# Kernel optimization log

Measured on AMD Instinct MI355X. Metric: run time of the kernel, lower is better.

## Reference

```python
import jax, jax.numpy as jnp
import numpy as np

H = 512  # hidden size (layer_size in the torch module)


def setup_inputs() -> dict:
    key = jax.random.key(0)
    ks = jax.random.split(key, 12)
    B, T = 512, 128
    s = 1.0 / np.sqrt(H)  # torch default LSTM/Linear init range
    def u(k, shape):
        return jax.random.uniform(k, shape, jnp.float32, -s, s)
    return {
        "x": jax.random.normal(ks[0], (B, T, 1), jnp.float32),
        "x_time": jax.random.normal(ks[1], (B, T), jnp.float32),
        "y_time": jax.random.normal(ks[2], (B, T), jnp.float32),
        # layer 0: input_size=1
        "w_ih0": u(ks[3], (4 * H, 1)),
        "w_hh0": u(ks[4], (4 * H, H)),
        "b_ih0": u(ks[5], (4 * H,)),
        "b_hh0": u(ks[6], (4 * H,)),
        # layer 1: input_size=H
        "w_ih1": u(ks[7], (4 * H, H)),
        "w_hh1": u(ks[8], (4 * H, H)),
        "b_ih1": u(ks[9], (4 * H,)),
        "b_hh1": u(ks[10], (4 * H,)),
        # output head Linear(512, 1)
        "w_lin": u(ks[11], (1, H)),
        "b_lin": jnp.zeros((1,), jnp.float32),
    }


def _cell(x, h, c, w_ih, w_hh, b):
    # torch LSTM gate order: i, f, g, o
    g = x @ w_ih.T + h @ w_hh.T + b
    i, f, gg, o = jnp.split(g, 4, axis=-1)
    c = jax.nn.sigmoid(f) * c + jax.nn.sigmoid(i) * jnp.tanh(gg)
    h = jax.nn.sigmoid(o) * jnp.tanh(c)
    return h, c


def reference(x, x_time, y_time, w_ih0, w_hh0, b_ih0, b_hh0,
              w_ih1, w_hh1, b_ih1, b_hh1, w_lin, b_lin):
    # x: [B, T, 1]; x_time / y_time are unused (as in the torch module)
    B, T, _ = x.shape
    b0 = b_ih0 + b_hh0
    b1 = b_ih1 + b_hh1

    def step(state, x_t):  # x_t: [B, 1]
        h1, c1, h2, c2 = state
        h1, c1 = _cell(x_t, h1, c1, w_ih0, w_hh0, b0)
        h2, c2 = _cell(h1, h2, c2, w_ih1, w_hh1, b1)
        return (h1, c1, h2, c2), h2

    z = jnp.zeros((B, H), x.dtype)
    state = (z, z, z, z)
    # phase 1: run the 2-layer LSTM over the full input sequence (first loop iter)
    state, _ = jax.lax.scan(step, state, jnp.swapaxes(x, 0, 1))
    y0 = state[3] @ w_lin.T + b_lin  # [B, 1] first prediction

    def ar_step(carry, _):
        st, y = carry
        st, h2 = step(st, y)
        y_new = h2 @ w_lin.T + b_lin
        return (st, y_new), y_new

    _, ys = jax.lax.scan(ar_step, (state, y0), None, length=T - 1)  # [T-1, B, 1]
    preds = jnp.concatenate([y0[None], ys], axis=0)  # [T, B, 1]
    return jnp.transpose(preds, (1, 0, 2))  # [B, T, 1]
```

## Files before the change

kernel.cpp:

```cpp
#include <hip/hip_runtime.h>
#include <math.h>
#include <stdint.h>


namespace {
constexpr int NH  = 512;
constexpr int NT  = 128;
constexpr int NB  = 512;
}

typedef __attribute__((ext_vector_type(8))) short bf16x8;
typedef __attribute__((ext_vector_type(4))) float f32x4;
typedef __attribute__((ext_vector_type(4))) unsigned int u32x4;

__global__ void ReLSTM_18940805775611_kernel() {}

__device__ __forceinline__ unsigned short lstm9_f2b(float f) {
    union { float f; uint32_t i; } v; v.f = f;
    const uint32_t r = v.i + 0x7FFFu + ((v.i >> 16) & 1u);
    return (unsigned short)(r >> 16);
}
__device__ __forceinline__ float lstm9_sig(float x) {
    return 1.0f / (1.0f + expf(-x));
}

__global__ void lstm9_mark(float* out) {
    const int i = blockIdx.x * blockDim.x + threadIdx.x;
    if (i < NB * NT) out[i] = 2.03125f;
}

__global__ void lstm9_prep(
    const float* whh0, const float* wih1, const float* whh1,
    const float* bih0, const float* bhh0, const float* bih1, const float* bhh1,
    unsigned short* wb0, unsigned short* wb1i, unsigned short* wb1h,
    float* bsum0, float* bsum1,
    unsigned short* hz, int* flags)
{
    const size_t stride = (size_t)gridDim.x * blockDim.x;
    const size_t i0 = (size_t)blockIdx.x * blockDim.x + threadIdx.x;
    const size_t NW = (size_t)4 * NH * NH;
    for (size_t i = i0; i < NW; i += stride) {
        wb0 [i] = lstm9_f2b(whh0[i]);
        wb1i[i] = lstm9_f2b(wih1[i]);
        wb1h[i] = lstm9_f2b(whh1[i]);
    }
    for (size_t i = i0; i < (size_t)4 * NH; i += stride) {
        bsum0[i] = bih0[i] + bhh0[i];
        bsum1[i] = bih1[i] + bhh1[i];
    }
    for (size_t i = i0; i < (size_t)4 * NB * NH; i += stride) hz[i] = 0;
    for (size_t i = i0; i < (size_t)2 * 256 * 8 * 32; i += stride) flags[i] = 0;
}

__device__ __forceinline__ void lstm9_ldA(u32x4& d, const unsigned short* p) {
    asm volatile("global_load_dwordx4 %0, %1, off sc0 sc1"
                 : "=v"(d) : "v"(p) : "memory");
}
__device__ __forceinline__ void lstm9_ldP(u32x4& d, const float* p) {
    asm volatile("global_load_dwordx4 %0, %1, off sc0 sc1"
                 : "=v"(d) : "v"(p) : "memory");
}
#define LSTM9_W8(N, a,b,c,d,e,f,g,h) \
    asm volatile("s_waitcnt vmcnt(" #N ")" \
        : "+v"(a),"+v"(b),"+v"(c),"+v"(d),"+v"(e),"+v"(f),"+v"(g),"+v"(h) :: "memory")
#define LSTM9_WAIT2(a,b) \
    asm volatile("s_waitcnt vmcnt(0)" : "+v"(a),"+v"(b) :: "memory")
__device__ __forceinline__ void lstm9_stH(unsigned short* p, unsigned short v) {
    unsigned int x = v;
    asm volatile("global_store_short %0, %1, off sc0 sc1" :: "v"(p), "v"(x) : "memory");
}
__device__ __forceinline__ void lstm9_stF(float* p, float v) {
    asm volatile("global_store_dword %0, %1, off sc0 sc1" :: "v"(p), "v"(v) : "memory");
}
__device__ __forceinline__ void lstm9_stI(int* p, int v) {
    asm volatile("global_store_dword %0, %1, off sc0 sc1" :: "v"(p), "v"(v) : "memory");
}
__device__ __forceinline__ void lstm9_drain() {
    asm volatile("s_waitcnt vmcnt(0)" ::: "memory");
}

__device__ __forceinline__ void lstm9_waitgrp(const int* base) {
    if (threadIdx.x < 64) {
        const int sl = (int)threadIdx.x & 31;
        int it = 0;
        for (;;) {
            int f;
            asm volatile("global_load_dword %0, %1, off sc0 sc1\n\t"
                         "s_waitcnt vmcnt(0)"
                         : "=v"(f) : "v"(base + sl) : "memory");
            if (__all(f != 0)) break;
            if (it < 4) __builtin_amdgcn_s_sleep(1);
            else        __builtin_amdgcn_s_sleep(8);
            ++it;
        }
    }
    __syncthreads();
}
__device__ __forceinline__ void lstm9_waitgrp2(const int* baseA, const int* baseB) {
    if (threadIdx.x < 64) {
        const int sl = (int)threadIdx.x & 31;
        const int* p = ((threadIdx.x < 32) ? baseA : baseB) + sl;
        int it = 0;
        for (;;) {
            int f;
            asm volatile("global_load_dword %0, %1, off sc0 sc1\n\t"
                         "s_waitcnt vmcnt(0)"
                         : "=v"(f) : "v"(p) : "memory");
            if (__all(f != 0)) break;
            if (it < 4) __builtin_amdgcn_s_sleep(1);
            else        __builtin_amdgcn_s_sleep(8);
            ++it;
        }
    }
    __syncthreads();
}

#define BFR0(gt, kk) (*(const bf16x8*)&Bsh0[gt][kk][lane][0])
#define BFR1(gt, kk) (*(const bf16x8*)&Bsh1[gt][kk][lane][0])
#define WHR(gt, kk)  (*(const bf16x8*)&whr[(gt) * 16 + (kk)])

#define LSTM9_L0_MFMAS()                                                          \
    do {                                                                          \
        _Pragma("unroll")                                                         \
        for (int ks = 0; ks < 8; ++ks) {                                          \
            const bf16x8 af = *(const bf16x8*)&rA1[ks];                           \
            a0 = __builtin_amdgcn_mfma_f32_16x16x32_bf16(af, BFR0(0, ks), a0, 0, 0, 0); \
            a1 = __builtin_amdgcn_mfma_f32_16x16x32_bf16(af, BFR0(1, ks), a1, 0, 0, 0); \
            a2 = __builtin_amdgcn_mfma_f32_16x16x32_bf16(af, BFR0(2, ks), a2, 0, 0, 0); \
            a3 = __builtin_amdgcn_mfma_f32_16x16x32_bf16(af, BFR0(3, ks), a3, 0, 0, 0); \
        }                                                                         \
        _Pragma("unroll")                                                         \
        for (int ks = 0; ks < 8; ++ks) {                                          \
            const bf16x8 af = *(const bf16x8*)&rA2[ks];                           \
            a0 = __builtin_amdgcn_mfma_f32_16x16x32_bf16(af, BFR0(0, 8 + ks), a0, 0, 0, 0); \
            a1 = __builtin_amdgcn_mfma_f32_16x16x32_bf16(af, BFR0(1, 8 + ks), a1, 0, 0, 0); \
            a2 = __builtin_amdgcn_mfma_f32_16x16x32_bf16(af, BFR0(2, 8 + ks), a2, 0, 0, 0); \
            a3 = __builtin_amdgcn_mfma_f32_16x16x32_bf16(af, BFR0(3, 8 + ks), a3, 0, 0, 0); \
        }                                                                         \
    } while (0)

__global__ __launch_bounds__(256, 1) void lstm9_persist(
    const float* __restrict__ xin, float* __restrict__ outf,
    const unsigned short* __restrict__ wb0,
    const unsigned short* __restrict__ wb1i,
    const unsigned short* __restrict__ wb1h,
    const float* __restrict__ bsum0, const float* __restrict__ bsum1,
    const float* __restrict__ wih0f, const float* __restrict__ wlinf,
    const float* __restrict__ blinf,
    unsigned short* h1a, unsigned short* h1b,
    unsigned short* h2a, unsigned short* h2b,
    float* parts, int* flags)
{
    __shared__ unsigned short Bsh0[4][16][64][8];
    __shared__ unsigned short Bsh1[4][16][64][8];
    __shared__ float redsh[64][17];
    __shared__ float ysh[64];

    const int tid  = threadIdx.x;
    const int lane = tid & 63;
    const int wv   = tid >> 6;
    const int quad = lane >> 4;
    const int ln15 = lane & 15;
    const int bid  = blockIdx.x;
    const int jt = (bid & 7) * 4 + ((bid >> 3) & 3);
    const int g  = bid >> 5;
    const int j0 = jt * 16;
    const int m0 = g * 64;
    const int rowA = m0 + wv * 16 + ln15;
    const int mb   = m0 + wv * 16 + quad * 4;
    const int jv   = j0 + ln15;

    for (int idx = tid; idx < 4 * 16 * 64; idx += 256) {
        const int gt = idx >> 10;
        const int ks = (idx >> 6) & 15;
        const int l  = idx & 63;
        const int row = l & 15, q = l >> 4;
        const size_t go = ((size_t)(gt * NH + j0 + row)) * NH + ks * 32 + q * 8;
        *(u32x4*)&Bsh0[gt][ks][l][0] = *(const u32x4*)(wb0  + go);
        *(u32x4*)&Bsh1[gt][ks][l][0] = *(const u32x4*)(wb1i + go);
    }
    u32x4 whr[64];
    #pragma unroll
    for (int gt = 0; gt < 4; ++gt) {
        #pragma unroll
        for (int ks = 0; ks < 16; ++ks)
            whr[gt * 16 + ks] = *(const u32x4*)(
                wb1h + ((size_t)(gt * NH + j0 + ln15)) * NH + ks * 32 + quad * 8);
    }
    __syncthreads();

    const float b0i = bsum0[jv],          b0f = bsum0[NH + jv];
    const float b0g = bsum0[2 * NH + jv], b0o = bsum0[3 * NH + jv];
    const float wxi = wih0f[jv],          wxf = wih0f[NH + jv];
    const float wxg = wih0f[2 * NH + jv], wxo = wih0f[3 * NH + jv];
    const float b1i = bsum1[jv],          b1f = bsum1[NH + jv];
    const float b1g = bsum1[2 * NH + jv], b1o = bsum1[3 * NH + jv];
    const float wl_ = wlinf[jv];
    const float bl_ = blinf[0];

    float c1r[4] = {0.f, 0.f, 0.f, 0.f};
    float c2r[4] = {0.f, 0.f, 0.f, 0.f};

    unsigned short* h1p[2] = { h1a, h1b };
    unsigned short* h2p[2] = { h2a, h2b };
    int* flagA = flags;
    int* flagB = flags + 256 * 8 * 32;

    u32x4 rA1[8], rA2[8];
    #pragma unroll
    for (int ks = 0; ks < 8; ++ks) {
        rA1[ks] = (u32x4){0u, 0u, 0u, 0u};
        rA2[ks] = (u32x4){0u, 0u, 0u, 0u};
    }
    u32x4 rH2a[8], rH2b[8];

    for (int t = 0; t < 256; ++t) {
        unsigned short*       h1wr = h1p[(t + 1) & 1];
        const unsigned short* h2rd = h2p[t & 1];
        unsigned short*       h2wr = h2p[(t + 1) & 1];

        float xv[4] = {0.f, 0.f, 0.f, 0.f};
        f32x4 a0 = {0.f, 0.f, 0.f, 0.f};
        f32x4 a1 = a0, a2 = a0, a3 = a0;
        if (t < 128) {
            #pragma unroll
            for (int r = 0; r < 4; ++r)
                xv[r] = xin[(size_t)(mb + r) * NT + t];
            LSTM9_L0_MFMAS();
        } else {
            lstm9_waitgrp(flagB + ((t - 1) * 8 + g) * 32);
            const float* pslot = parts + (size_t)((t - 1) & 1) * NB * 32;
            const int row = tid >> 2, q = tid & 3;
            u32x4 v0, v1;
            lstm9_ldP(v0, pslot + (size_t)(m0 + row) * 32 + q * 8);
            lstm9_ldP(v1, pslot + (size_t)(m0 + row) * 32 + q * 8 + 4);
            if (t < 255) LSTM9_L0_MFMAS();
            LSTM9_WAIT2(v0, v1);
            const float* f0 = (const float*)&v0;
            const float* f1 = (const float*)&v1;
            redsh[row][q] = f0[0] + f0[1] + f0[2] + f0[3]
                          + f1[0] + f1[1] + f1[2] + f1[3];
            __syncthreads();
            if (tid < 64) {
                const float y = bl_ + redsh[tid][0] + redsh[tid][1]
                                    + redsh[tid][2] + redsh[tid][3];
                ysh[tid] = y;
                if (jt == 0)
                    outf[(size_t)(m0 + tid) * NT + (t - 128)] = y;
            }
            __syncthreads();
            if (t == 255) break;
            #pragma unroll
            for (int r = 0; r < 4; ++r)
                xv[r] = ysh[wv * 16 + quad * 4 + r];
        }

        #pragma unroll
        for (int r = 0; r < 4; ++r) {
            const float gi = a0[r] + fmaf(xv[r], wxi, b0i);
            const float gf = a1[r] + fmaf(xv[r], wxf, b0f);
            const float gg = a2[r] + fmaf(xv[r], wxg, b0g);
            const float go = a3[r] + fmaf(xv[r], wxo, b0o);
            float cv = c1r[r];
            cv = lstm9_sig(gf) * cv + lstm9_sig(gi) * tanhf(gg);
            c1r[r] = cv;
            lstm9_stH(h1wr + (size_t)(mb + r) * NH + jv,
                      lstm9_f2b(lstm9_sig(go) * tanhf(cv)));
        }
        lstm9_drain();
        __syncthreads();
        if (tid == 0) lstm9_stI(flagA + (t * 8 + g) * 32 + jt, 1);

        if (t < 128) {
            const int* bA = flagA + (t * 8 + g) * 32;
            const int* bB = (t >= 1) ? (flagB + ((t - 1) * 8 + g) * 32) : bA;
            lstm9_waitgrp2(bA, bB);
        } else {
            lstm9_waitgrp(flagA + (t * 8 + g) * 32);
        }

        a0 = {0.f, 0.f, 0.f, 0.f}; a1 = a0; a2 = a0; a3 = a0;
        #pragma unroll
        for (int ks = 0; ks < 8; ++ks)
            lstm9_ldA(rH2a[ks], h2rd + (size_t)rowA * NH + ks * 32 + quad * 8);
        #pragma unroll
        for (int ks = 0; ks < 8; ++ks)
            lstm9_ldA(rH2b[ks], h2rd + (size_t)rowA * NH + (8 + ks) * 32 + quad * 8);
        #pragma unroll
        for (int ks = 0; ks < 8; ++ks)
            lstm9_ldA(rA1[ks], h1wr + (size_t)rowA * NH + ks * 32 + quad * 8);
        #pragma unroll
        for (int ks = 0; ks < 8; ++ks)
            lstm9_ldA(rA2[ks], h1wr + (size_t)rowA * NH + (8 + ks) * 32 + quad * 8);

        LSTM9_W8(24, rH2a[0], rH2a[1], rH2a[2], rH2a[3],
                     rH2a[4], rH2a[5], rH2a[6], rH2a[7]);
        #pragma unroll
        for (int ks = 0; ks < 8; ++ks) {
            const bf16x8 af = *(const bf16x8*)&rH2a[ks];
            a0 = __builtin_amdgcn_mfma_f32_16x16x32_bf16(af, WHR(0, ks), a0, 0, 0, 0);
            a1 = __builtin_amdgcn_mfma_f32_16x16x32_bf16(af, WHR(1, ks), a1, 0, 0, 0);
            a2 = __builtin_amdgcn_mfma_f32_16x16x32_bf16(af, WHR(2, ks), a2, 0, 0, 0);
            a3 = __builtin_amdgcn_mfma_f32_16x16x32_bf16(af, WHR(3, ks), a3, 0, 0, 0);
        }
        LSTM9_W8(16, rH2b[0], rH2b[1], rH2b[2], rH2b[3],
                     rH2b[4], rH2b[5], rH2b[6], rH2b[7]);
        #pragma unroll
        for (int ks = 0; ks < 8; ++ks) {
            const bf16x8 af = *(const bf16x8*)&rH2b[ks];
            a0 = __builtin_amdgcn_mfma_f32_16x16x32_bf16(af, WHR(0, 8 + ks), a0, 0, 0, 0);
            a1 = __builtin_amdgcn_mfma_f32_16x16x32_bf16(af, WHR(1, 8 + ks), a1, 0, 0, 0);
            a2 = __builtin_amdgcn_mfma_f32_16x16x32_bf16(af, WHR(2, 8 + ks), a2, 0, 0, 0);
            a3 = __builtin_amdgcn_mfma_f32_16x16x32_bf16(af, WHR(3, 8 + ks), a3, 0, 0, 0);
        }
        LSTM9_W8(8, rA1[0], rA1[1], rA1[2], rA1[3],
                    rA1[4], rA1[5], rA1[6], rA1[7]);
        #pragma unroll
        for (int ks = 0; ks < 8; ++ks) {
            const bf16x8 af = *(const bf16x8*)&rA1[ks];
            a0 = __builtin_amdgcn_mfma_f32_16x16x32_bf16(af, BFR1(0, ks), a0, 0, 0, 0);
            a1 = __builtin_amdgcn_mfma_f32_16x16x32_bf16(af, BFR1(1, ks), a1, 0, 0, 0);
            a2 = __builtin_amdgcn_mfma_f32_16x16x32_bf16(af, BFR1(2, ks), a2, 0, 0, 0);
            a3 = __builtin_amdgcn_mfma_f32_16x16x32_bf16(af, BFR1(3, ks), a3, 0, 0, 0);
        }
        LSTM9_W8(0, rA2[0], rA2[1], rA2[2], rA2[3],
                    rA2[4], rA2[5], rA2[6], rA2[7]);
        #pragma unroll
        for (int ks = 0; ks < 8; ++ks) {
            const bf16x8 af = *(const bf16x8*)&rA2[ks];
            a0 = __builtin_amdgcn_mfma_f32_16x16x32_bf16(af, BFR1(0, 8 + ks), a0, 0, 0, 0);
            a1 = __builtin_amdgcn_mfma_f32_16x16x32_bf16(af, BFR1(1, 8 + ks), a1, 0, 0, 0);
            a2 = __builtin_amdgcn_mfma_f32_16x16x32_bf16(af, BFR1(2, 8 + ks), a2, 0, 0, 0);
            a3 = __builtin_amdgcn_mfma_f32_16x16x32_bf16(af, BFR1(3, 8 + ks), a3, 0, 0, 0);
        }

        float hv[4], cva[4];
        #pragma unroll
        for (int r = 0; r < 4; ++r) {
            const float gi = a0[r] + b1i;
            const float gf = a1[r] + b1f;
            const float gg = a2[r] + b1g;
            const float go = a3[r] + b1o;
            float cv = c2r[r];
            cv = lstm9_sig(gf) * cv + lstm9_sig(gi) * tanhf(gg);
            c2r[r] = cv;
            cva[r] = cv;
            hv[r] = lstm9_sig(go) * tanhf(cv);
            lstm9_stH(h2wr + (size_t)(mb + r) * NH + jv, lstm9_f2b(hv[r]));
        }
        if (t >= 127) {
            #pragma unroll
            for (int r = 0; r < 4; ++r)
                redsh[wv * 16 + quad * 4 + r][ln15] =
                    (t == 127 ? cva[r] : hv[r]) * wl_;
            __syncthreads();
            if (tid < 64) {
                float s = 0.0f;
                #pragma unroll
                for (int j = 0; j < 16; ++j) s += redsh[tid][j];
                lstm9_stF(parts + (size_t)(t & 1) * NB * 32
                                + (size_t)(m0 + tid) * 32 + jt, s);
            }
        }
        lstm9_drain();
        __syncthreads();
        if (tid == 0) lstm9_stI(flagB + (t * 8 + g) * 32 + jt, 1);
    }
}

extern "C" void kernel_launch(void* const* d_in, const int* in_sizes, int n_in,
                              void* d_out, int out_size, void* d_ws, size_t ws_size,
                              hipStream_t stream)
{
    int base = 3;
    if (!(n_in > 3 && in_sizes[3] == 4 * NH)) {
        for (int i = 1; i + 9 < n_in; ++i)
            if (in_sizes[i] == 4 * NH) { base = i; break; }
    }
    const float* xin  = (const float*)d_in[0];
    const float* wih0 = (const float*)d_in[base + 0];
    const float* whh0 = (const float*)d_in[base + 1];
    const float* bih0 = (const float*)d_in[base + 2];
    const float* bhh0 = (const float*)d_in[base + 3];
    const float* wih1 = (const float*)d_in[base + 4];
    const float* whh1 = (const float*)d_in[base + 5];
    const float* bih1 = (const float*)d_in[base + 6];
    const float* bhh1 = (const float*)d_in[base + 7];
    const float* wlin = (const float*)d_in[base + 8];
    const float* blin = (const float*)d_in[base + 9];
    float* outf = (float*)d_out;

    const size_t NW = (size_t)4 * NH * NH;
    const size_t S  = (size_t)NB * NH;
    unsigned short* wb0  = (unsigned short*)d_ws;
    unsigned short* wb1i = wb0 + NW;
    unsigned short* wb1h = wb1i + NW;
    unsigned short* h1b0 = wb1h + NW;
    unsigned short* h1b1 = h1b0 + S;
    unsigned short* h2b0 = h1b1 + S;
    unsigned short* h2b1 = h2b0 + S;
    float* bsum0 = (float*)(h2b1 + S);
    float* bsum1 = bsum0 + 4 * NH;
    float* parts = bsum1 + 4 * NH;
    int*   flags = (int*)(parts + 2 * NB * 32);

    lstm9_mark<<<(NB * NT + 255) / 256, 256, 0, stream>>>(outf);
    lstm9_prep<<<1024, 256, 0, stream>>>(whh0, wih1, whh1, bih0, bhh0, bih1, bhh1,
                                         wb0, wb1i, wb1h, bsum0, bsum1,
                                         h1b0, flags);
    lstm9_persist<<<256, 256, 0, stream>>>(xin, outf, wb0, wb1i, wb1h,
                                           bsum0, bsum1, wih0, wlin, blin,
                                           h1b0, h1b1, h2b0, h2b1,
                                           parts, flags);
}
```

Before: 3.409 ms.

## Restructure persistent LSTM loop to merge layer-0 and layer-1 barriers per step

Reorders the persistent kernel's time loop so each iteration waits once for both h1(t) and h2(t-1), runs layer 1, then computes layer 0 for the next step. In the teacher-forced phase both flags are published together, which removes one grid-wide wait per timestep. The layer-0 epilogue becomes a macro and the first layer-0 step is peeled out before the loop. The autoregressive phase keeps a separate wait on the partial-sum flags. The flag protocol is now more intricate and carries a risk of ordering bugs.

Result: faster. 3.076 ms (-9.8%).

```diff
diff --git a/kernel.cpp b/kernel.cpp
--- a/kernel.cpp
+++ b/kernel.cpp
@@ -124,18 +124,34 @@
         _Pragma("unroll")                                                         \
         for (int ks = 0; ks < 8; ++ks) {                                          \
             const bf16x8 af = *(const bf16x8*)&rA1[ks];                           \
-            a0 = __builtin_amdgcn_mfma_f32_16x16x32_bf16(af, BFR0(0, ks), a0, 0, 0, 0); \
-            a1 = __builtin_amdgcn_mfma_f32_16x16x32_bf16(af, BFR0(1, ks), a1, 0, 0, 0); \
-            a2 = __builtin_amdgcn_mfma_f32_16x16x32_bf16(af, BFR0(2, ks), a2, 0, 0, 0); \
-            a3 = __builtin_amdgcn_mfma_f32_16x16x32_bf16(af, BFR0(3, ks), a3, 0, 0, 0); \
+            b0 = __builtin_amdgcn_mfma_f32_16x16x32_bf16(af, BFR0(0, ks), b0, 0, 0, 0); \
+            b1 = __builtin_amdgcn_mfma_f32_16x16x32_bf16(af, BFR0(1, ks), b1, 0, 0, 0); \
+            b2 = __builtin_amdgcn_mfma_f32_16x16x32_bf16(af, BFR0(2, ks), b2, 0, 0, 0); \
+            b3 = __builtin_amdgcn_mfma_f32_16x16x32_bf16(af, BFR0(3, ks), b3, 0, 0, 0); \
         }                                                                         \
         _Pragma("unroll")                                                         \
         for (int ks = 0; ks < 8; ++ks) {                                          \
             const bf16x8 af = *(const bf16x8*)&rA2[ks];                           \
-            a0 = __builtin_amdgcn_mfma_f32_16x16x32_bf16(af, BFR0(0, 8 + ks), a0, 0, 0, 0); \
-            a1 = __builtin_amdgcn_mfma_f32_16x16x32_bf16(af, BFR0(1, 8 + ks), a1, 0, 0, 0); \
-            a2 = __builtin_amdgcn_mfma_f32_16x16x32_bf16(af, BFR0(2, 8 + ks), a2, 0, 0, 0); \
-            a3 = __builtin_amdgcn_mfma_f32_16x16x32_bf16(af, BFR0(3, 8 + ks), a3, 0, 0, 0); \
+            b0 = __builtin_amdgcn_mfma_f32_16x16x32_bf16(af, BFR0(0, 8 + ks), b0, 0, 0, 0); \
+            b1 = __builtin_amdgcn_mfma_f32_16x16x32_bf16(af, BFR0(1, 8 + ks), b1, 0, 0, 0); \
+            b2 = __builtin_amdgcn_mfma_f32_16x16x32_bf16(af, BFR0(2, 8 + ks), b2, 0, 0, 0); \
+            b3 = __builtin_amdgcn_mfma_f32_16x16x32_bf16(af, BFR0(3, 8 + ks), b3, 0, 0, 0); \
+        }                                                                         \
+    } while (0)
+
+#define LSTM9_L0_EPI(h1dst)                                                       \
+    do {                                                                          \
+        _Pragma("unroll")                                                         \
+        for (int r = 0; r < 4; ++r) {                                             \
+            const float gi = b0[r] + fmaf(xv[r], wxi, b0i);                       \
+            const float gf = b1[r] + fmaf(xv[r], wxf, b0f);                       \
+            const float gg = b2[r] + fmaf(xv[r], wxg, b0g);                       \
+            const float go = b3[r] + fmaf(xv[r], wxo, b0o);                       \
+            float cv = c1r[r];                                                    \
+            cv = lstm9_sig(gf) * cv + lstm9_sig(gi) * tanhf(gg);                  \
+            c1r[r] = cv;                                                          \
+            lstm9_stH((h1dst) + (size_t)(mb + r) * NH + jv,                       \
+                      lstm9_f2b(lstm9_sig(go) * tanhf(cv)));                      \
         }                                                                         \
     } while (0)
 
@@ -206,93 +222,46 @@
     int* flagA = flags;
     int* flagB = flags + 256 * 8 * 32;
 
-    u32x4 rA1[8], rA2[8];
-    #pragma unroll
-    for (int ks = 0; ks < 8; ++ks) {
-        rA1[ks] = (u32x4){0u, 0u, 0u, 0u};
-        rA2[ks] = (u32x4){0u, 0u, 0u, 0u};
-    }
-    u32x4 rH2a[8], rH2b[8];
-
-    for (int t = 0; t < 256; ++t) {
-        unsigned short*       h1wr = h1p[(t + 1) & 1];
+    u32x4 rA1[8], rA2[8], rH2a[8], rH2b[8];
+
+    {
+        float xv[4];
+        f32x4 b0 = {0.f, 0.f, 0.f, 0.f};
+        f32x4 b1 = b0, b2 = b0, b3 = b0;
+        #pragma unroll
+        for (int r = 0; r < 4; ++r)
+            xv[r] = xin[(size_t)(mb + r) * NT + 0];
+        LSTM9_L0_EPI(h1p[1]);
+        lstm9_drain();
+        __syncthreads();
+        if (tid == 0) lstm9_stI(flagA + (0 * 8 + g) * 32 + jt, 1);
+    }
+
+    for (int t = 0; t < 255; ++t) {
+        const unsigned short* h1rd = h1p[(t + 1) & 1];
+        unsigned short*       h1wr = h1p[t & 1];
         const unsigned short* h2rd = h2p[t & 1];
         unsigned short*       h2wr = h2p[(t + 1) & 1];
 
-        float xv[4] = {0.f, 0.f, 0.f, 0.f};
+        if (t == 0) lstm9_waitgrp(flagA + (0 * 8 + g) * 32);
+        else        lstm9_waitgrp2(flagA + (t * 8 + g) * 32,
+                                   flagB + ((t - 1) * 8 + g) * 32);
+
+        #pragma unroll
+        for (int ks = 0; ks < 8; ++ks)
+            lstm9_ldA(rH2a[ks], h2rd + (size_t)rowA * NH + ks * 32 + quad * 8);
+        #pragma unroll
+        for (int ks = 0; ks < 8; ++ks)
+            lstm9_ldA(rH2b[ks], h2rd + (size_t)rowA * NH + (8 + ks) * 32 + quad * 8);
+        #pragma unroll
+        for (int ks = 0; ks < 8; ++ks)
+            lstm9_ldA(rA1[ks], h1rd + (size_t)rowA * NH + ks * 32 + quad * 8);
+        #pragma unroll
+        for (int ks = 0; ks < 8; ++ks)
+            lstm9_ldA(rA2[ks], h1rd + (size_t)rowA * NH + (8 + ks) * 32 + quad * 8);
+
         f32x4 a0 = {0.f, 0.f, 0.f, 0.f};
         f32x4 a1 = a0, a2 = a0, a3 = a0;
-        if (t < 128) {
-            #pragma unroll
-            for (int r = 0; r < 4; ++r)
-                xv[r] = xin[(size_t)(mb + r) * NT + t];
-            LSTM9_L0_MFMAS();
-        } else {
-            lstm9_waitgrp(flagB + ((t - 1) * 8 + g) * 32);
-            const float* pslot = parts + (size_t)((t - 1) & 1) * NB * 32;
-            const int row = tid >> 2, q = tid & 3;
-            u32x4 v0, v1;
-            lstm9_ldP(v0, pslot + (size_t)(m0 + row) * 32 + q * 8);
-            lstm9_ldP(v1, pslot + (size_t)(m0 + row) * 32 + q * 8 + 4);
-            if (t < 255) LSTM9_L0_MFMAS();
-            LSTM9_WAIT2(v0, v1);
-            const float* f0 = (const float*)&v0;
-            const float* f1 = (const float*)&v1;
-            redsh[row][q] = f0[0] + f0[1] + f0[2] + f0[3]
-                          + f1[0] + f1[1] + f1[2] + f1[3];
-            __syncthreads();
-            if (tid < 64) {
-                const float y = bl_ + redsh[tid][0] + redsh[tid][1]
-                                    + redsh[tid][2] + redsh[tid][3];
-                ysh[tid] = y;
-                if (jt == 0)
-                    outf[(size_t)(m0 + tid) * NT + (t - 128)] = y;
-            }
-            __syncthreads();
-            if (t == 255) break;
-            #pragma unroll
-            for (int r = 0; r < 4; ++r)
-                xv[r] = ysh[wv * 16 + quad * 4 + r];
-        }
-
-        #pragma unroll
-        for (int r = 0; r < 4; ++r) {
-            const float gi = a0[r] + fmaf(xv[r], wxi, b0i);
-            const float gf = a1[r] + fmaf(xv[r], wxf, b0f);
-            const float gg = a2[r] + fmaf(xv[r], wxg, b0g);
-            const float go = a3[r] + fmaf(xv[r], wxo, b0o);
-            float cv = c1r[r];
-            cv = lstm9_sig(gf) * cv + lstm9_sig(gi) * tanhf(gg);
-            c1r[r] = cv;
-            lstm9_stH(h1wr + (size_t)(mb + r) * NH + jv,
-                      lstm9_f2b(lstm9_sig(go) * tanhf(cv)));
-        }
-        lstm9_drain();
-        __syncthreads();
-        if (tid == 0) lstm9_stI(flagA + (t * 8 + g) * 32 + jt, 1);
-
-        if (t < 128) {
-            const int* bA = flagA + (t * 8 + g) * 32;
-            const int* bB = (t >= 1) ? (flagB + ((t - 1) * 8 + g) * 32) : bA;
-            lstm9_waitgrp2(bA, bB);
-        } else {
-            lstm9_waitgrp(flagA + (t * 8 + g) * 32);
-        }
-
-        a0 = {0.f, 0.f, 0.f, 0.f}; a1 = a0; a2 = a0; a3 = a0;
-        #pragma unroll
-        for (int ks = 0; ks < 8; ++ks)
-            lstm9_ldA(rH2a[ks], h2rd + (size_t)rowA * NH + ks * 32 + quad * 8);
-        #pragma unroll
-        for (int ks = 0; ks < 8; ++ks)
-            lstm9_ldA(rH2b[ks], h2rd + (size_t)rowA * NH + (8 + ks) * 32 + quad * 8);
-        #pragma unroll
-        for (int ks = 0; ks < 8; ++ks)
-            lstm9_ldA(rA1[ks], h1wr + (size_t)rowA * NH + ks * 32 + quad * 8);
-        #pragma unroll
-        for (int ks = 0; ks < 8; ++ks)
-            lstm9_ldA(rA2[ks], h1wr + (size_t)rowA * NH + (8 + ks) * 32 + quad * 8);
-
         LSTM9_W8(24, rH2a[0], rH2a[1], rH2a[2], rH2a[3],
                      rH2a[4], rH2a[5], rH2a[6], rH2a[7]);
         #pragma unroll
@@ -348,7 +317,24 @@
             hv[r] = lstm9_sig(go) * tanhf(cv);
             lstm9_stH(h2wr + (size_t)(mb + r) * NH + jv, lstm9_f2b(hv[r]));
         }
-        if (t >= 127) {
+
+        f32x4 b0 = {0.f, 0.f, 0.f, 0.f};
+        f32x4 b1 = b0, b2 = b0, b3 = b0;
+
+        if (t < 127) {
+            LSTM9_L0_MFMAS();
+            float xv[4];
+            #pragma unroll
+            for (int r = 0; r < 4; ++r)
+                xv[r] = xin[(size_t)(mb + r) * NT + (t + 1)];
+            LSTM9_L0_EPI(h1wr);
+            lstm9_drain();
+            __syncthreads();
+            if (tid == 0) {
+                lstm9_stI(flagB + (t * 8 + g) * 32 + jt, 1);
+                lstm9_stI(flagA + ((t + 1) * 8 + g) * 32 + jt, 1);
+            }
+        } else {
             #pragma unroll
             for (int r = 0; r < 4; ++r)
                 redsh[wv * 16 + quad * 4 + r][ln15] =
@@ -361,10 +347,45 @@
                 lstm9_stF(parts + (size_t)(t & 1) * NB * 32
                                 + (size_t)(m0 + tid) * 32 + jt, s);
             }
-        }
-        lstm9_drain();
-        __syncthreads();
-        if (tid == 0) lstm9_stI(flagB + (t * 8 + g) * 32 + jt, 1);
+            lstm9_drain();
+            __syncthreads();
+            if (tid == 0) lstm9_stI(flagB + (t * 8 + g) * 32 + jt, 1);
+
+            if (t < 254) LSTM9_L0_MFMAS();
+
+            lstm9_waitgrp(flagB + (t * 8 + g) * 32);
+            const float* pslot = parts + (size_t)(t & 1) * NB * 32;
+            {
+                const int row = tid >> 2, q = tid & 3;
+                u32x4 v0, v1;
+                lstm9_ldP(v0, pslot + (size_t)(m0 + row) * 32 + q * 8);
+                lstm9_ldP(v1, pslot + (size_t)(m0 + row) * 32 + q * 8 + 4);
+                LSTM9_WAIT2(v0, v1);
+                const float* f0 = (const float*)&v0;
+                const float* f1 = (const float*)&v1;
+                redsh[row][q] = f0[0] + f0[1] + f0[2] + f0[3]
+                              + f1[0] + f1[1] + f1[2] + f1[3];
+            }
+            __syncthreads();
+            if (tid < 64) {
+                const float y = bl_ + redsh[tid][0] + redsh[tid][1]
+                                    + redsh[tid][2] + redsh[tid][3];
+                ysh[tid] = y;
+                if (jt == 0)
+                    outf[(size_t)(m0 + tid) * NT + (t - 127)] = y;
+            }
+            __syncthreads();
+            if (t == 254) break;
+
+            float xv[4];
+            #pragma unroll
+            for (int r = 0; r < 4; ++r)
+                xv[r] = ysh[wv * 16 + quad * 4 + r];
+            LSTM9_L0_EPI(h1wr);
+            lstm9_drain();
+            __syncthreads();
+            if (tid == 0) lstm9_stI(flagA + ((t + 1) * 8 + g) * 32 + jt, 1);
+        }
     }
 }
 
```
